# Kernel tuning notes

Measured on AMD Instinct MI355X. Metric: run time of the kernel, lower is better.

The kernel has to match this reference:

```python
import math
import jax, jax.numpy as jnp
import numpy as np

B, C, H, W = 32, 256, 32, 32  # in==mid==out channels

def setup_inputs() -> dict:
    key = jax.random.key(0)
    ks = jax.random.split(key, 3)
    x = jax.random.normal(ks[0], (B, C, H, W), dtype=jnp.float32)
    # 1x1 convs are just channel matmuls: weight [out_ch, in_ch]
    w_in = jax.random.normal(ks[1], (3 * C, C), dtype=jnp.float32) * (1.0 / math.sqrt(C))
    b_in = jnp.zeros((3 * C,), dtype=jnp.float32)
    # project_out has init_scale=0.0 in the original; we use random weights so the
    # output (and gradients) are non-trivial, but the math is identical.
    w_out = jax.random.normal(ks[2], (C, C), dtype=jnp.float32) * (1.0 / math.sqrt(C))
    b_out = jnp.zeros((C,), dtype=jnp.float32)
    return {"x": x, "w_in": w_in, "b_in": b_in, "w_out": w_out, "b_out": b_out}

def _qkv_attention(q, k, v):
    # q,k,v: [B,C,H,W]. Full spatial self-attention over the HxW grid.
    b, c, h, w = q.shape
    scores = jnp.einsum('bchw,bcHW->bhwHW', q, k)          # [B,H,W,H,W]
    scores = scores.reshape(b, h, w, h * w) / math.sqrt(c)
    attn = jax.nn.softmax(scores, axis=-1).reshape(b, h, w, h, w)
    return jnp.einsum('bhwHW,bcHW->bchw', attn, v)          # [B,C,H,W]

def reference(x, w_in, b_in, w_out, b_out):
    skip = x  # in_channels == out_channels -> Identity skip
    qkv = jnp.einsum('oc,bchw->bohw', w_in, x) + b_in[None, :, None, None]
    q, k, v = jnp.split(qkv, 3, axis=1)
    h = _qkv_attention(q, k, v)
    out = jnp.einsum('oc,bchw->bohw', w_out, h) + b_out[None, :, None, None]
    return out + skip
```

## Files before the change

kernel.cpp:

```cpp
#include <hip/hip_runtime.h>
#include <hip/hip_bf16.h>

typedef __attribute__((ext_vector_type(8))) short bf16x8;
typedef __attribute__((ext_vector_type(4))) float f32x4;
typedef __attribute__((ext_vector_type(16))) float f32x16;
typedef long long i64;

#define NB 32
#define NC 256
#define NN 1024

__device__ __forceinline__ unsigned pack2(float a, float b) {
    __hip_bfloat16 ha = __float2bfloat16(a), hb = __float2bfloat16(b);
    unsigned short ua = *(unsigned short*)&ha, ub = *(unsigned short*)&hb;
    return (unsigned)ua | ((unsigned)ub << 16);
}

__device__ __forceinline__ float bflo(unsigned u) {
    union { unsigned i; float f; } x; x.i = u << 16; return x.f;
}
__device__ __forceinline__ float bfhi(unsigned u) {
    union { unsigned i; float f; } x; x.i = u & 0xffff0000u; return x.f;
}
__device__ __forceinline__ unsigned fp8x4(float a, float b, float c, float d) {
    int w = __builtin_amdgcn_cvt_pk_fp8_f32(a, b, 0, false);
    w = __builtin_amdgcn_cvt_pk_fp8_f32(c, d, w, true);
    return (unsigned)w;
}

__device__ __forceinline__ void glds16(const void* g, void* lds) {
    __builtin_amdgcn_global_load_lds(
        (const __attribute__((address_space(1))) unsigned int*)g,
        (__attribute__((address_space(3))) unsigned int*)lds, 16, 0, 0);
}

__global__ __launch_bounds__(256) void xpose_kernel(
    const float* __restrict__ x, unsigned char* __restrict__ Xt8)
{
    __shared__ float Ls[64 * 67];
    const int t = threadIdx.x;
    const int n0 = blockIdx.x * 64, c0 = blockIdx.y * 64, b = blockIdx.z;
    const int cl = t >> 4, nl = (t & 15) * 4;
    const float* xb = x + ((size_t)b * NC + c0) * NN + n0;
    #pragma unroll
    for (int q4 = 0; q4 < 4; ++q4) {
        const int c = cl + q4 * 16;
        const float4 v = *(const float4*)(xb + (size_t)c * NN + nl);
        Ls[(nl + 0) * 67 + c] = v.x;
        Ls[(nl + 1) * 67 + c] = v.y;
        Ls[(nl + 2) * 67 + c] = v.z;
        Ls[(nl + 3) * 67 + c] = v.w;
    }
    __syncthreads();
    #pragma unroll
    for (int p = 0; p < 2; ++p) {
        const int idx = p * 256 + t, n = idx >> 3, cs = idx & 7;
        const float* r = &Ls[n * 67 + cs * 8];
        uint2 o;
        o.x = fp8x4(r[0], r[1], r[2], r[3]);
        o.y = fp8x4(r[4], r[5], r[6], r[7]);
        *(uint2*)(Xt8 + ((size_t)b * NN + n0 + n) * 256 + c0 + cs * 8) = o;
    }
}

__device__ __forceinline__ void stage_ab8(const unsigned char* __restrict__ Ag,
                                          const float* __restrict__ Bg,
                                          char* Ad, char* Bd, int ks, int t)
{
    #pragma unroll
    for (int p = 0; p < 2; ++p) {
        const int idx = p * 256 + t;
        const int row = idx >> 2, pc = idx & 3;
        const int lp = pc ^ (row & 3);
        glds16(Ag + (size_t)row * 256 + ks * 64 + lp * 16, Ad + idx * 16);
        const float* wp = Bg + (size_t)row * NC + ks * 64 + lp * 16;
        const float4 u0 = *(const float4*)wp;
        const float4 u1 = *(const float4*)(wp + 4);
        const float4 u2 = *(const float4*)(wp + 8);
        const float4 u3 = *(const float4*)(wp + 12);
        uint4 pk;
        pk.x = fp8x4(u0.x, u0.y, u0.z, u0.w);
        pk.y = fp8x4(u1.x, u1.y, u1.z, u1.w);
        pk.z = fp8x4(u2.x, u2.y, u2.z, u2.w);
        pk.w = fp8x4(u3.x, u3.y, u3.z, u3.w);
        *(uint4*)(Bd + idx * 16) = pk;
    }
}

__global__ __launch_bounds__(256, 3) void qkv_gemm_kernel(
    const unsigned char* __restrict__ Xt8, const float* __restrict__ w_in,
    const float* __restrict__ b_in, unsigned char* __restrict__ Qt8,
    unsigned char* __restrict__ Kt8, unsigned char* __restrict__ Vf8)
{
    __shared__ char smem[34816];
    char* const A0 = smem;
    char* const A1 = smem + 8192;
    char* const B0 = smem + 16384;
    char* const B1 = smem + 24576;

    const int t  = threadIdx.x;
    const int wv = t >> 6, ln = t & 63, lo = ln & 15, hi = ln >> 4;
    const int wm = wv >> 1, wn = wv & 1;
    const int n0 = blockIdx.x * 128, o0 = blockIdx.y * 128, b = blockIdx.z;

    const unsigned char* Ag = Xt8 + ((size_t)b * NN + n0) * 256;
    const float* Bg = w_in + (size_t)o0 * NC;

    f32x4 acc[4][4];
    #pragma unroll
    for (int i = 0; i < 4; ++i)
        #pragma unroll
        for (int j = 0; j < 4; ++j) acc[i][j] = (f32x4){0.f, 0.f, 0.f, 0.f};

    int ra[4], rb[4];
    #pragma unroll
    for (int f = 0; f < 4; ++f) { ra[f] = wm * 64 + f * 16 + lo; rb[f] = wn * 64 + f * 16 + lo; }

    stage_ab8(Ag, Bg, A0, B0, 0, t);
    __syncthreads();
    #pragma unroll
    for (int ks = 0; ks < 4; ++ks) {
        char* Ac = (ks & 1) ? A1 : A0;
        char* Bc = (ks & 1) ? B1 : B0;
        if (ks < 3)
            stage_ab8(Ag, Bg, (ks & 1) ? A0 : A1, (ks & 1) ? B0 : B1, ks + 1, t);
        #pragma unroll
        for (int kk = 0; kk < 2; ++kk) {
            i64 av[4], bv[4];
            #pragma unroll
            for (int f = 0; f < 4; ++f) {
                av[f] = *(const i64*)(Ac + ra[f] * 64 + (((kk << 2) | hi) ^ ((ra[f] & 3) << 1)) * 8);
                bv[f] = *(const i64*)(Bc + rb[f] * 64 + (((kk << 2) | hi) ^ ((rb[f] & 3) << 1)) * 8);
            }
            #pragma unroll
            for (int fm = 0; fm < 4; ++fm)
                #pragma unroll
                for (int fn = 0; fn < 4; ++fn)
                    acc[fm][fn] = __builtin_amdgcn_mfma_f32_16x16x32_fp8_fp8(
                        av[fm], bv[fn], acc[fm][fn], 0, 0, 0);
        }
        __syncthreads();
    }

    float bias[4];
    #pragma unroll
    for (int fn = 0; fn < 4; ++fn) bias[fn] = b_in[o0 + wn * 64 + fn * 16 + lo];

    __hip_bfloat16* Ls = (__hip_bfloat16*)smem;
    if (o0 < 512) {
        #pragma unroll
        for (int fm = 0; fm < 4; ++fm)
            #pragma unroll
            for (int fn = 0; fn < 4; ++fn)
                #pragma unroll
                for (int r = 0; r < 4; ++r)
                    Ls[(wm * 64 + fm * 16 + hi * 4 + r) * 136 + wn * 64 + fn * 16 + lo] =
                        __float2bfloat16(acc[fm][fn][r] + bias[fn]);
        __syncthreads();
        unsigned char* dst = (o0 < 256) ? Qt8 : Kt8;
        const int oc = (o0 < 256) ? o0 : o0 - 256;
        #pragma unroll
        for (int p = 0; p < 4; ++p) {
            const int idx = p * 256 + t, row = idx >> 3, ch = idx & 7;
            const unsigned* ls = (const unsigned*)&Ls[row * 136 + ch * 16];
            const uint4 a = *(const uint4*)ls;
            const uint4 b2 = *(const uint4*)(ls + 4);
            uint4 o;
            o.x = fp8x4(bflo(a.x), bfhi(a.x), bflo(a.y), bfhi(a.y));
            o.y = fp8x4(bflo(a.z), bfhi(a.z), bflo(a.w), bfhi(a.w));
            o.z = fp8x4(bflo(b2.x), bfhi(b2.x), bflo(b2.y), bfhi(b2.y));
            o.w = fp8x4(bflo(b2.z), bfhi(b2.z), bflo(b2.w), bfhi(b2.w));
            *(uint4*)(dst + ((size_t)b * NN + n0 + row) * 256 + oc + ch * 16) = o;
        }
    } else {
        #pragma unroll
        for (int fm = 0; fm < 4; ++fm)
            #pragma unroll
            for (int fn = 0; fn < 4; ++fn)
                #pragma unroll
                for (int r = 0; r < 4; ++r)
                    Ls[(wn * 64 + fn * 16 + lo) * 136 + wm * 64 + fm * 16 + hi * 4 + r] =
                        __float2bfloat16(acc[fm][fn][r] + bias[fn]);
        __syncthreads();
        #pragma unroll
        for (int p = 0; p < 8; ++p) {
            const int idx = p * 256 + t;
            const int ch = idx >> 7, cr = idx & 127;
            const unsigned* ls = (const unsigned*)&Ls[cr * 136 + ch * 8];
            const uint4 a = *(const uint4*)ls;
            uint2 o;
            o.x = fp8x4(bflo(a.x), bfhi(a.x), bflo(a.y), bfhi(a.y));
            o.y = fp8x4(bflo(a.z), bfhi(a.z), bflo(a.w), bfhi(a.w));
            const int g = (n0 >> 3) + ch;
            *(uint2*)(Vf8 + (((size_t)b * 128 + g) * 256 + (o0 - 512) + cr) * 8) = o;
        }
    }
}

__device__ __forceinline__ void stage_tile(const unsigned char* __restrict__ Kb,
                                           const unsigned char* __restrict__ Vb,
                                           char* Kd, char* Vd, int m0, int t)
{
    {
        const int row = t >> 4, pc = t & 15;
        const int prow = (row & 19) | ((row & 4) << 1) | ((row & 8) >> 1);
        const int sc = pc ^ (row & 15);
        glds16(Kb + (size_t)(m0 + prow) * 256 + sc * 16, Kd + t * 16);
    }
    {
        glds16(Vb + (size_t)(m0 >> 3) * 2048 + t * 16, Vd + t * 16);
    }
}

__global__ __launch_bounds__(512, 2) void attn_kernel(
    const unsigned char* __restrict__ Qt8, const unsigned char* __restrict__ Kt8,
    const unsigned char* __restrict__ Vf8, const float* __restrict__ w_out,
    const float* __restrict__ b_out, const float* __restrict__ xg,
    float* __restrict__ out)
{
    __shared__ char smem[139264];

    const int t  = threadIdx.x;
    const int wv = t >> 6, ln = t & 63;
    const int l32 = ln & 31, h2 = ln >> 5;
    const int qgrp = wv & 3, half = wv >> 2;
    const int wid = blockIdx.x + 8 * blockIdx.y;
    const int swz = (wid & 7) * 32 + (wid >> 3);
    const int qb = swz & 7, b = swz >> 3;
    const int n0 = qb * 128;
    const float scale = 0.0625f;

    const unsigned char* Kbase = Kt8 + (size_t)b * NN * 256;
    const unsigned char* Vbase = Vf8 + (size_t)b * 128 * 2048;

    const unsigned char* qp = Qt8 + ((size_t)b * NN + n0 + qgrp * 32 + l32) * 256;
    i64 qf[16];
    #pragma unroll
    for (int ks = 0; ks < 16; ++ks)
        qf[ks] = *(const i64*)(qp + ks * 16 + h2 * 8);

    f32x16 acc[8];
    #pragma unroll
    for (int ct = 0; ct < 8; ++ct)
        #pragma unroll
        for (int r = 0; r < 16; ++r) acc[ct][r] = 0.f;
    float mr = 0.f;
    float sr = 0.f;

    #pragma unroll
    for (int tt = 0; tt < 4; ++tt)
        stage_tile(Kbase, Vbase, smem + tt * 8192,
                   smem + 65536 + tt * 8192, tt * 32, t);

    for (int s = 0; s < 16; ++s) {
        if (s < 14) {
            const int t2 = 2 * s + 4, t3 = 2 * s + 5;
            stage_tile(Kbase, Vbase, smem + (t2 & 7) * 8192,
                       smem + 65536 + (t2 & 7) * 8192, t2 * 32, t);
            stage_tile(Kbase, Vbase, smem + (t3 & 7) * 8192,
                       smem + 65536 + (t3 & 7) * 8192, t3 * 32, t);
        }
        if (s <= 13)      asm volatile("s_waitcnt vmcnt(8)" ::: "memory");
        else if (s == 14) asm volatile("s_waitcnt vmcnt(4)" ::: "memory");
        else              asm volatile("s_waitcnt vmcnt(0)" ::: "memory");
        __builtin_amdgcn_s_barrier();
        __builtin_amdgcn_sched_barrier(0);

        const int tile = 2 * s + half;
        char* const Kc = smem + (tile & 7) * 8192;
        char* const Vc = smem + 65536 + (tile & 7) * 8192;

        f32x16 sfA, sfB;
        #pragma unroll
        for (int r = 0; r < 16; ++r) { sfA[r] = 0.f; sfB[r] = 0.f; }
        __builtin_amdgcn_s_setprio(1);
        #pragma unroll
        for (int ks = 0; ks < 8; ++ks) {
            const int pc = ks ^ (l32 & 15);
            const i64 kf = *(const i64*)(Kc + l32 * 256 + pc * 16 + h2 * 8);
            sfA = __builtin_amdgcn_mfma_f32_32x32x16_fp8_fp8(kf, qf[ks], sfA, 0, 0, 0);
        }
        #pragma unroll
        for (int ks = 8; ks < 16; ++ks) {
            const int pc = ks ^ (l32 & 15);
            const i64 kf = *(const i64*)(Kc + l32 * 256 + pc * 16 + h2 * 8);
            sfB = __builtin_amdgcn_mfma_f32_32x32x16_fp8_fp8(kf, qf[ks], sfB, 0, 0, 0);
        }
        __builtin_amdgcn_s_setprio(0);

        float sv[16];
        #pragma unroll
        for (int r = 0; r < 16; ++r) sv[r] = sfA[r] + sfB[r];

        float m0a = fmaxf(sv[0], sv[1]),  m1a = fmaxf(sv[2], sv[3]);
        float m2a = fmaxf(sv[4], sv[5]),  m3a = fmaxf(sv[6], sv[7]);
        float m4a = fmaxf(sv[8], sv[9]),  m5a = fmaxf(sv[10], sv[11]);
        float m6a = fmaxf(sv[12], sv[13]), m7a = fmaxf(sv[14], sv[15]);
        float m0b = fmaxf(m0a, m1a), m1b = fmaxf(m2a, m3a);
        float m2b = fmaxf(m4a, m5a), m3b = fmaxf(m6a, m7a);
        float tm = fmaxf(fmaxf(m0b, m1b), fmaxf(m2b, m3b));
        tm = fmaxf(tm, __shfl_xor(tm, 32, 64));
        tm *= scale;
        if (__any(tm > mr + 8.f)) {
            const float mn = fmaxf(mr, tm);
            const float al = __expf(mr - mn);
            mr = mn;
            sr *= al;
            #pragma unroll
            for (int ct = 0; ct < 8; ++ct)
                #pragma unroll
                for (int r = 0; r < 16; ++r) acc[ct][r] *= al;
        }
        float p[16];
        #pragma unroll
        for (int r = 0; r < 16; ++r)
            p[r] = __expf(sv[r] * scale - mr);
        float s0a = p[0] + p[1],  s1a = p[2] + p[3];
        float s2a = p[4] + p[5],  s3a = p[6] + p[7];
        float s4a = p[8] + p[9],  s5a = p[10] + p[11];
        float s6a = p[12] + p[13], s7a = p[14] + p[15];
        float sacc = ((s0a + s1a) + (s2a + s3a)) + ((s4a + s5a) + (s6a + s7a));
        sacc += __shfl_xor(sacc, 32, 64);
        sr += sacc;

        i64 pb[2];
        #pragma unroll
        for (int kstep = 0; kstep < 2; ++kstep) {
            union { unsigned u[2]; i64 l; } uu;
            uu.u[0] = fp8x4(p[8 * kstep + 0], p[8 * kstep + 1],
                            p[8 * kstep + 2], p[8 * kstep + 3]);
            uu.u[1] = fp8x4(p[8 * kstep + 4], p[8 * kstep + 5],
                            p[8 * kstep + 6], p[8 * kstep + 7]);
            pb[kstep] = uu.l;
        }

        __builtin_amdgcn_s_setprio(1);
        #pragma unroll
        for (int ct = 0; ct < 8; ++ct) {
            #pragma unroll
            for (int kstep = 0; kstep < 2; ++kstep) {
                const i64 vf = *(const i64*)(Vc + (2 * kstep + h2) * 2048 +
                                             (ct * 32 + l32) * 8);
                acc[ct] = __builtin_amdgcn_mfma_f32_32x32x16_fp8_fp8(vf, pb[kstep], acc[ct], 0, 0, 0);
            }
        }
        __builtin_amdgcn_s_setprio(0);
    }
    __syncthreads();

    float* const ex = (float*)smem;
    __hip_bfloat16* const Hld = (__hip_bfloat16*)(smem + 69632);
    #pragma unroll
    for (int ph = 0; ph < 2; ++ph) {
        if (half == 1 && (qgrp >> 1) == ph) {
            float* dst = ex + ((qgrp & 1) * 64 + ln) * 132;
            #pragma unroll
            for (int ct = 0; ct < 8; ++ct)
                #pragma unroll
                for (int rr = 0; rr < 4; ++rr) {
                    f32x4 v = {acc[ct][rr * 4 + 0], acc[ct][rr * 4 + 1],
                               acc[ct][rr * 4 + 2], acc[ct][rr * 4 + 3]};
                    *(f32x4*)(dst + ct * 16 + rr * 4) = v;
                }
            dst[128] = mr;
            dst[129] = sr;
        }
        __syncthreads();
        if (half == 0 && (qgrp >> 1) == ph) {
            const float* src = ex + ((qgrp & 1) * 64 + ln) * 132;
            const float mb = src[128], lb = src[129];
            const float m = fmaxf(mr, mb);
            float fa = __expf(mr - m), fb = __expf(mb - m);
            const float inv = 1.0f / (sr * fa + lb * fb);
            fa *= inv; fb *= inv;
            __hip_bfloat16* hrow = Hld + (size_t)(qgrp * 32 + l32) * 264;
            #pragma unroll
            for (int ct = 0; ct < 8; ++ct)
                #pragma unroll
                for (int ss = 0; ss < 4; ++ss) {
                    const float o0 = acc[ct][ss * 4 + 0] * fa + src[ct * 16 + ss * 4 + 0] * fb;
                    const float o1 = acc[ct][ss * 4 + 1] * fa + src[ct * 16 + ss * 4 + 1] * fb;
                    const float o2 = acc[ct][ss * 4 + 2] * fa + src[ct * 16 + ss * 4 + 2] * fb;
                    const float o3 = acc[ct][ss * 4 + 3] * fa + src[ct * 16 + ss * 4 + 3] * fb;
                    uint2 v;
                    v.x = pack2(o0, o1);
                    v.y = pack2(o2, o3);
                    *(uint2*)(hrow + ct * 32 + ss * 8 + h2 * 4) = v;
                }
        }
        __syncthreads();
    }

    __hip_bfloat16* const Wld = (__hip_bfloat16*)smem;
    const int oT = wv >> 1;
    const int nT0 = (wv & 1) * 2, nT1 = nT0 + 1;
    for (int oh = 0; oh < 2; ++oh) {
        #pragma unroll
        for (int p = 0; p < 8; ++p) {
            const int idx = p * 512 + t;
            const int o = idx >> 5, ck = idx & 31;
            const float* wp = w_out + (size_t)(oh * 128 + o) * NC + ck * 8;
            const float4 u0 = *(const float4*)wp;
            const float4 u1 = *(const float4*)(wp + 4);
            uint4 pk;
            pk.x = pack2(u0.x, u0.y); pk.y = pack2(u0.z, u0.w);
            pk.z = pack2(u1.x, u1.y); pk.w = pack2(u1.z, u1.w);
            *(uint4*)((char*)Wld + (size_t)o * 528 + ck * 16) = pk;
        }
        __syncthreads();

        f32x16 oc0, oc1;
        #pragma unroll
        for (int r = 0; r < 16; ++r) { oc0[r] = 0.f; oc1[r] = 0.f; }
        __builtin_amdgcn_s_setprio(1);
        #pragma unroll
        for (int ks = 0; ks < 16; ++ks) {
            const int ck = ks * 2 + h2;
            bf16x8 wf = *(const bf16x8*)((char*)Wld + (size_t)(oT * 32 + l32) * 528 + ck * 16);
            bf16x8 hf0 = *(const bf16x8*)((char*)Hld + (size_t)(nT0 * 32 + l32) * 528 + ck * 16);
            bf16x8 hf1 = *(const bf16x8*)((char*)Hld + (size_t)(nT1 * 32 + l32) * 528 + ck * 16);
            oc0 = __builtin_amdgcn_mfma_f32_32x32x16_bf16(wf, hf0, oc0, 0, 0, 0);
            oc1 = __builtin_amdgcn_mfma_f32_32x32x16_bf16(wf, hf1, oc1, 0, 0, 0);
        }
        __builtin_amdgcn_s_setprio(0);

        #pragma unroll
        for (int r = 0; r < 16; ++r) {
            const int o = oh * 128 + oT * 32 + (r & 3) + 8 * (r >> 2) + 4 * h2;
            const float bo = b_out[o];
            const size_t rowg = ((size_t)b * NC + o) * NN + n0;
            const size_t g0 = rowg + nT0 * 32 + l32;
            const size_t g1 = rowg + nT1 * 32 + l32;
            out[g0] = oc0[r] + bo + xg[g0];
            out[g1] = oc1[r] + bo + xg[g1];
        }
        __syncthreads();
    }
}

extern "C" void kernel_launch(void* const* d_in, const int* in_sizes, int n_in,
                              void* d_out, int out_size, void* d_ws, size_t ws_size,
                              hipStream_t stream) {
    const float* x     = (const float*)d_in[0];
    const float* w_in  = (const float*)d_in[1];
    const float* b_in  = (const float*)d_in[2];
    const float* w_out = (const float*)d_in[3];
    const float* b_out = (const float*)d_in[4];
    float* out = (float*)d_out;

    if (ws_size < (size_t)32 * 1024 * 1024) return;
    char* ws = (char*)d_ws;
    unsigned char* Qt8 = (unsigned char*)(ws);
    unsigned char* Kt8 = (unsigned char*)(ws + ((size_t)8 << 20));
    unsigned char* Vf8 = (unsigned char*)(ws + ((size_t)16 << 20));
    unsigned char* Xt8 = (unsigned char*)(ws + ((size_t)24 << 20));

    xpose_kernel<<<dim3(16, 4, 32), 256, 0, stream>>>(x, Xt8);
    qkv_gemm_kernel<<<dim3(8, 6, 32), 256, 0, stream>>>(Xt8, w_in, b_in, Qt8, Kt8, Vf8);
    attn_kernel<<<dim3(8, 32), 512, 0, stream>>>(Qt8, Kt8, Vf8, w_out, b_out, x, out);
}
```

Baseline: 85.16 us.

## Fuse x transpose/fp8 conversion into QKV GEMM with resident A panel

Removes the separate transpose kernel and its Xt8 workspace. Each block now loads a 128-position slice of x through LDS, transposes it and converts it to fp8 into a resident 32KB swizzled A panel. It then loops over three 128-wide output tiles, reusing that panel. This saves one launch and a global round trip of the transposed activations. In exchange the grid shrinks from 1536 to 512 blocks, LDS use grows to about 66KB per block (occupancy 2), and the transpose phase is serialized before the GEMM.

```diff
diff --git a/kernel.cpp b/kernel.cpp
--- a/kernel.cpp
+++ b/kernel.cpp
@@ -34,166 +34,170 @@
         (__attribute__((address_space(3))) unsigned int*)lds, 16, 0, 0);
 }
 
-__global__ __launch_bounds__(256) void xpose_kernel(
-    const float* __restrict__ x, unsigned char* __restrict__ Xt8)
-{
-    __shared__ float Ls[64 * 67];
-    const int t = threadIdx.x;
-    const int n0 = blockIdx.x * 64, c0 = blockIdx.y * 64, b = blockIdx.z;
-    const int cl = t >> 4, nl = (t & 15) * 4;
-    const float* xb = x + ((size_t)b * NC + c0) * NN + n0;
-    #pragma unroll
-    for (int q4 = 0; q4 < 4; ++q4) {
-        const int c = cl + q4 * 16;
-        const float4 v = *(const float4*)(xb + (size_t)c * NN + nl);
-        Ls[(nl + 0) * 67 + c] = v.x;
-        Ls[(nl + 1) * 67 + c] = v.y;
-        Ls[(nl + 2) * 67 + c] = v.z;
-        Ls[(nl + 3) * 67 + c] = v.w;
-    }
-    __syncthreads();
-    #pragma unroll
-    for (int p = 0; p < 2; ++p) {
-        const int idx = p * 256 + t, n = idx >> 3, cs = idx & 7;
-        const float* r = &Ls[n * 67 + cs * 8];
-        uint2 o;
-        o.x = fp8x4(r[0], r[1], r[2], r[3]);
-        o.y = fp8x4(r[4], r[5], r[6], r[7]);
-        *(uint2*)(Xt8 + ((size_t)b * NN + n0 + n) * 256 + c0 + cs * 8) = o;
-    }
-}
-
-__device__ __forceinline__ void stage_ab8(const unsigned char* __restrict__ Ag,
-                                          const float* __restrict__ Bg,
-                                          char* Ad, char* Bd, int ks, int t)
-{
-    #pragma unroll
-    for (int p = 0; p < 2; ++p) {
-        const int idx = p * 256 + t;
-        const int row = idx >> 2, pc = idx & 3;
-        const int lp = pc ^ (row & 3);
-        glds16(Ag + (size_t)row * 256 + ks * 64 + lp * 16, Ad + idx * 16);
-        const float* wp = Bg + (size_t)row * NC + ks * 64 + lp * 16;
-        const float4 u0 = *(const float4*)wp;
-        const float4 u1 = *(const float4*)(wp + 4);
-        const float4 u2 = *(const float4*)(wp + 8);
-        const float4 u3 = *(const float4*)(wp + 12);
-        uint4 pk;
-        pk.x = fp8x4(u0.x, u0.y, u0.z, u0.w);
-        pk.y = fp8x4(u1.x, u1.y, u1.z, u1.w);
-        pk.z = fp8x4(u2.x, u2.y, u2.z, u2.w);
-        pk.w = fp8x4(u3.x, u3.y, u3.z, u3.w);
-        *(uint4*)(Bd + idx * 16) = pk;
-    }
-}
-
-__global__ __launch_bounds__(256, 3) void qkv_gemm_kernel(
-    const unsigned char* __restrict__ Xt8, const float* __restrict__ w_in,
+__global__ __launch_bounds__(256, 2) void qkv_panel_kernel(
+    const float* __restrict__ x, const float* __restrict__ w_in,
     const float* __restrict__ b_in, unsigned char* __restrict__ Qt8,
     unsigned char* __restrict__ Kt8, unsigned char* __restrict__ Vf8)
 {
-    __shared__ char smem[34816];
-    char* const A0 = smem;
-    char* const A1 = smem + 8192;
-    char* const B0 = smem + 16384;
-    char* const B1 = smem + 24576;
+    __shared__ char smem[67584];
+    char* const Ap = smem;
+    char* const X0 = smem + 32768;
+    char* const X1 = smem + 49152;
+    char* const B0 = smem + 32768;
+    char* const B1 = smem + 40960;
+    __hip_bfloat16* const Ls = (__hip_bfloat16*)(smem + 32768);
 
     const int t  = threadIdx.x;
     const int wv = t >> 6, ln = t & 63, lo = ln & 15, hi = ln >> 4;
     const int wm = wv >> 1, wn = wv & 1;
-    const int n0 = blockIdx.x * 128, o0 = blockIdx.y * 128, b = blockIdx.z;
-
-    const unsigned char* Ag = Xt8 + ((size_t)b * NN + n0) * 256;
-    const float* Bg = w_in + (size_t)o0 * NC;
-
-    f32x4 acc[4][4];
-    #pragma unroll
-    for (int i = 0; i < 4; ++i)
-        #pragma unroll
-        for (int j = 0; j < 4; ++j) acc[i][j] = (f32x4){0.f, 0.f, 0.f, 0.f};
+    const int n0 = blockIdx.x * 128, og = blockIdx.y, b = blockIdx.z;
+    const float* xb = x + (size_t)b * NC * NN;
+
+    auto xstage = [&](int cc, char* Xd) {
+        #pragma unroll
+        for (int p2 = 0; p2 < 4; ++p2) {
+            const int idx = p2 * 256 + t;
+            const int r = idx >> 5, u = idx & 31;
+            glds16(xb + (size_t)(cc * 32 + r) * NN + n0 + u * 4, Xd + idx * 16);
+        }
+    };
+    const int tn = t & 127, thalf = t >> 7;
+    auto xpose_chunk = [&](int cc, const char* Xd) {
+        const float* Xf = (const float*)Xd;
+        float v[16];
+        #pragma unroll
+        for (int j = 0; j < 16; ++j) v[j] = Xf[(thalf * 16 + j) * 128 + tn];
+        uint4 pk;
+        pk.x = fp8x4(v[0],  v[1],  v[2],  v[3]);
+        pk.y = fp8x4(v[4],  v[5],  v[6],  v[7]);
+        pk.z = fp8x4(v[8],  v[9],  v[10], v[11]);
+        pk.w = fp8x4(v[12], v[13], v[14], v[15]);
+        const int m = cc * 2 + thalf;
+        *(uint4*)(Ap + tn * 256 + (m ^ (tn & 7)) * 16) = pk;
+    };
+
+    xstage(0, X0);
+    __syncthreads();
+    for (int cc = 0; cc < 8; ++cc) {
+        char* cur = (cc & 1) ? X1 : X0;
+        if (cc < 7) xstage(cc + 1, (cc & 1) ? X0 : X1);
+        xpose_chunk(cc, cur);
+        __syncthreads();
+    }
+
+    auto bstage = [&](int ot, int ks, char* Bd) {
+        #pragma unroll
+        for (int p2 = 0; p2 < 2; ++p2) {
+            const int idx = p2 * 256 + t;
+            const int row = idx >> 2, pc = idx & 3;
+            const int lp = pc ^ (row & 3);
+            const float* wp = w_in + (size_t)(ot * 128 + row) * NC + ks * 64 + lp * 16;
+            const float4 u0 = *(const float4*)wp;
+            const float4 u1 = *(const float4*)(wp + 4);
+            const float4 u2 = *(const float4*)(wp + 8);
+            const float4 u3 = *(const float4*)(wp + 12);
+            uint4 pk;
+            pk.x = fp8x4(u0.x, u0.y, u0.z, u0.w);
+            pk.y = fp8x4(u1.x, u1.y, u1.z, u1.w);
+            pk.z = fp8x4(u2.x, u2.y, u2.z, u2.w);
+            pk.w = fp8x4(u3.x, u3.y, u3.z, u3.w);
+            *(uint4*)(Bd + idx * 16) = pk;
+        }
+    };
 
     int ra[4], rb[4];
     #pragma unroll
     for (int f = 0; f < 4; ++f) { ra[f] = wm * 64 + f * 16 + lo; rb[f] = wn * 64 + f * 16 + lo; }
 
-    stage_ab8(Ag, Bg, A0, B0, 0, t);
-    __syncthreads();
-    #pragma unroll
-    for (int ks = 0; ks < 4; ++ks) {
-        char* Ac = (ks & 1) ? A1 : A0;
-        char* Bc = (ks & 1) ? B1 : B0;
-        if (ks < 3)
-            stage_ab8(Ag, Bg, (ks & 1) ? A0 : A1, (ks & 1) ? B0 : B1, ks + 1, t);
-        #pragma unroll
-        for (int kk = 0; kk < 2; ++kk) {
-            i64 av[4], bv[4];
-            #pragma unroll
-            for (int f = 0; f < 4; ++f) {
-                av[f] = *(const i64*)(Ac + ra[f] * 64 + (((kk << 2) | hi) ^ ((ra[f] & 3) << 1)) * 8);
-                bv[f] = *(const i64*)(Bc + rb[f] * 64 + (((kk << 2) | hi) ^ ((rb[f] & 3) << 1)) * 8);
+    for (int ot3 = 0; ot3 < 3; ++ot3) {
+        const int ot = og * 3 + ot3;
+        const int o0 = ot * 128;
+
+        f32x4 acc[4][4];
+        #pragma unroll
+        for (int i = 0; i < 4; ++i)
+            #pragma unroll
+            for (int j = 0; j < 4; ++j) acc[i][j] = (f32x4){0.f, 0.f, 0.f, 0.f};
+
+        bstage(ot, 0, B0);
+        __syncthreads();
+        #pragma unroll
+        for (int ks = 0; ks < 4; ++ks) {
+            char* Bc = (ks & 1) ? B1 : B0;
+            if (ks < 3) bstage(ot, ks + 1, (ks & 1) ? B0 : B1);
+            #pragma unroll
+            for (int kk = 0; kk < 2; ++kk) {
+                const int c8 = (kk << 2) | hi;
+                const int m16 = ks * 4 + (c8 >> 1), h8 = c8 & 1;
+                i64 av[4], bv[4];
+                #pragma unroll
+                for (int f = 0; f < 4; ++f) {
+                    av[f] = *(const i64*)(Ap + ra[f] * 256 + ((m16 ^ (ra[f] & 7)) * 16) + h8 * 8);
+                    bv[f] = *(const i64*)(Bc + rb[f] * 64 + ((c8 ^ ((rb[f] & 3) << 1))) * 8);
+                }
+                #pragma unroll
+                for (int fm = 0; fm < 4; ++fm)
+                    #pragma unroll
+                    for (int fn = 0; fn < 4; ++fn)
+                        acc[fm][fn] = __builtin_amdgcn_mfma_f32_16x16x32_fp8_fp8(
+                            av[fm], bv[fn], acc[fm][fn], 0, 0, 0);
             }
+            __syncthreads();
+        }
+
+        float bias[4];
+        #pragma unroll
+        for (int fn = 0; fn < 4; ++fn) bias[fn] = b_in[o0 + wn * 64 + fn * 16 + lo];
+
+        if (o0 < 512) {
             #pragma unroll
             for (int fm = 0; fm < 4; ++fm)
                 #pragma unroll
                 for (int fn = 0; fn < 4; ++fn)
-                    acc[fm][fn] = __builtin_amdgcn_mfma_f32_16x16x32_fp8_fp8(
-                        av[fm], bv[fn], acc[fm][fn], 0, 0, 0);
-        }
-        __syncthreads();
-    }
-
-    float bias[4];
-    #pragma unroll
-    for (int fn = 0; fn < 4; ++fn) bias[fn] = b_in[o0 + wn * 64 + fn * 16 + lo];
-
-    __hip_bfloat16* Ls = (__hip_bfloat16*)smem;
-    if (o0 < 512) {
-        #pragma unroll
-        for (int fm = 0; fm < 4; ++fm)
-            #pragma unroll
-            for (int fn = 0; fn < 4; ++fn)
-                #pragma unroll
-                for (int r = 0; r < 4; ++r)
-                    Ls[(wm * 64 + fm * 16 + hi * 4 + r) * 136 + wn * 64 + fn * 16 + lo] =
-                        __float2bfloat16(acc[fm][fn][r] + bias[fn]);
-        __syncthreads();
-        unsigned char* dst = (o0 < 256) ? Qt8 : Kt8;
-        const int oc = (o0 < 256) ? o0 : o0 - 256;
-        #pragma unroll
-        for (int p = 0; p < 4; ++p) {
-            const int idx = p * 256 + t, row = idx >> 3, ch = idx & 7;
-            const unsigned* ls = (const unsigned*)&Ls[row * 136 + ch * 16];
-            const uint4 a = *(const uint4*)ls;
-            const uint4 b2 = *(const uint4*)(ls + 4);
-            uint4 o;
-            o.x = fp8x4(bflo(a.x), bfhi(a.x), bflo(a.y), bfhi(a.y));
-            o.y = fp8x4(bflo(a.z), bfhi(a.z), bflo(a.w), bfhi(a.w));
-            o.z = fp8x4(bflo(b2.x), bfhi(b2.x), bflo(b2.y), bfhi(b2.y));
-            o.w = fp8x4(bflo(b2.z), bfhi(b2.z), bflo(b2.w), bfhi(b2.w));
-            *(uint4*)(dst + ((size_t)b * NN + n0 + row) * 256 + oc + ch * 16) = o;
-        }
-    } else {
-        #pragma unroll
-        for (int fm = 0; fm < 4; ++fm)
-            #pragma unroll
-            for (int fn = 0; fn < 4; ++fn)
-                #pragma unroll
-                for (int r = 0; r < 4; ++r)
-                    Ls[(wn * 64 + fn * 16 + lo) * 136 + wm * 64 + fm * 16 + hi * 4 + r] =
-                        __float2bfloat16(acc[fm][fn][r] + bias[fn]);
-        __syncthreads();
-        #pragma unroll
-        for (int p = 0; p < 8; ++p) {
-            const int idx = p * 256 + t;
-            const int ch = idx >> 7, cr = idx & 127;
-            const unsigned* ls = (const unsigned*)&Ls[cr * 136 + ch * 8];
-            const uint4 a = *(const uint4*)ls;
-            uint2 o;
-            o.x = fp8x4(bflo(a.x), bfhi(a.x), bflo(a.y), bfhi(a.y));
-            o.y = fp8x4(bflo(a.z), bfhi(a.z), bflo(a.w), bfhi(a.w));
-            const int g = (n0 >> 3) + ch;
-            *(uint2*)(Vf8 + (((size_t)b * 128 + g) * 256 + (o0 - 512) + cr) * 8) = o;
-        }
+                    #pragma unroll
+                    for (int r = 0; r < 4; ++r)
+                        Ls[(wm * 64 + fm * 16 + hi * 4 + r) * 136 + wn * 64 + fn * 16 + lo] =
+                            __float2bfloat16(acc[fm][fn][r] + bias[fn]);
+            __syncthreads();
+            unsigned char* dst = (o0 < 256) ? Qt8 : Kt8;
+            const int oc = (o0 < 256) ? o0 : o0 - 256;
+            #pragma unroll
+            for (int p = 0; p < 4; ++p) {
+                const int idx = p * 256 + t, row = idx >> 3, ch = idx & 7;
+                const unsigned* ls = (const unsigned*)&Ls[row * 136 + ch * 16];
+                const uint4 a = *(const uint4*)ls;
+                const uint4 b2 = *(const uint4*)(ls + 4);
+                uint4 o;
+                o.x = fp8x4(bflo(a.x), bfhi(a.x), bflo(a.y), bfhi(a.y));
+                o.y = fp8x4(bflo(a.z), bfhi(a.z), bflo(a.w), bfhi(a.w));
+                o.z = fp8x4(bflo(b2.x), bfhi(b2.x), bflo(b2.y), bfhi(b2.y));
+                o.w = fp8x4(bflo(b2.z), bfhi(b2.z), bflo(b2.w), bfhi(b2.w));
+                *(uint4*)(dst + ((size_t)b * NN + n0 + row) * 256 + oc + ch * 16) = o;
+            }
+        } else {
+            #pragma unroll
+            for (int fm = 0; fm < 4; ++fm)
+                #pragma unroll
+                for (int fn = 0; fn < 4; ++fn)
+                    #pragma unroll
+                    for (int r = 0; r < 4; ++r)
+                        Ls[(wn * 64 + fn * 16 + lo) * 136 + wm * 64 + fm * 16 + hi * 4 + r] =
+                            __float2bfloat16(acc[fm][fn][r] + bias[fn]);
+            __syncthreads();
+            #pragma unroll
+            for (int p = 0; p < 8; ++p) {
+                const int idx = p * 256 + t;
+                const int ch = idx >> 7, cr = idx & 127;
+                const unsigned* ls = (const unsigned*)&Ls[cr * 136 + ch * 8];
+                const uint4 a = *(const uint4*)ls;
+                uint2 o;
+                o.x = fp8x4(bflo(a.x), bfhi(a.x), bflo(a.y), bfhi(a.y));
+                o.y = fp8x4(bflo(a.z), bfhi(a.z), bflo(a.w), bfhi(a.w));
+                const int g = (n0 >> 3) + ch;
+                *(uint2*)(Vf8 + (((size_t)b * 128 + g) * 256 + (o0 - 512) + cr) * 8) = o;
+            }
+        }
+        __syncthreads();
     }
 }
 
@@ -448,14 +452,12 @@
     const float* b_out = (const float*)d_in[4];
     float* out = (float*)d_out;
 
-    if (ws_size < (size_t)32 * 1024 * 1024) return;
+    if (ws_size < (size_t)24 * 1024 * 1024) return;
     char* ws = (char*)d_ws;
     unsigned char* Qt8 = (unsigned char*)(ws);
     unsigned char* Kt8 = (unsigned char*)(ws + ((size_t)8 << 20));
     unsigned char* Vf8 = (unsigned char*)(ws + ((size_t)16 << 20));
-    unsigned char* Xt8 = (unsigned char*)(ws + ((size_t)24 << 20));
-
-    xpose_kernel<<<dim3(16, 4, 32), 256, 0, stream>>>(x, Xt8);
-    qkv_gemm_kernel<<<dim3(8, 6, 32), 256, 0, stream>>>(Xt8, w_in, b_in, Qt8, Kt8, Vf8);
+
+    qkv_panel_kernel<<<dim3(8, 2, 32), 256, 0, stream>>>(x, w_in, b_in, Qt8, Kt8, Vf8);
     attn_kernel<<<dim3(8, 32), 512, 0, stream>>>(Qt8, Kt8, Vf8, w_out, b_out, x, out);
 }
```

After: 83.78 us (median of 2 runs). Within noise of the previous version (-1.6%).
